# Kernel tuning notes

Measured on AMD Instinct MI355X. Metric: run time of the kernel, lower is better.

## Reference

```python
import jax, jax.numpy as jnp
import numpy as np

B, T, D, H = 32, 1024, 768, 768

def setup_inputs() -> dict:
    key = jax.random.key(0)
    k0, k1, k2, k3 = jax.random.split(key, 4)
    inputs = jax.random.normal(k0, (B, T, D), dtype=jnp.float32)
    # packed-sequence lengths: sorted descending, in [1, T]
    lengths = jnp.sort(jax.random.randint(k1, (B,), 1, T + 1))[::-1]
    # parameters (orthogonal-block init approximated by scaled gaussian)
    W_in = jax.random.normal(k2, (6 * H, D), dtype=jnp.float32) / np.sqrt(D)
    b_in = jnp.zeros((6 * H,), dtype=jnp.float32)
    W_s = jax.random.normal(k3, (5 * H, H), dtype=jnp.float32) / np.sqrt(H)
    # state bias: forget-gate block initialized to 1.0, rest 0
    b_s = jnp.zeros((5 * H,), dtype=jnp.float32).at[H:2 * H].set(1.0)
    return {"inputs": inputs, "W_in": W_in, "b_in": b_in,
            "W_s": W_s, "b_s": b_s, "lengths": lengths}

def reference(inputs, W_in, b_in, W_s, b_s, lengths):
    Bb, Tt, Dd = inputs.shape
    Hh = W_s.shape[1]
    # precompute all input projections in one big GEMM: [B,T,6H]
    proj_in = jnp.einsum('btd,kd->btk', inputs, W_in) + b_in
    mask = jnp.arange(Tt)[None, :] < lengths[:, None]  # [B,T] valid timesteps

    def step(carry, xs):
        h, c = carry                    # [B,H] each
        pi, m = xs                      # pi: [B,6H], m: [B] bool
        ps = h @ W_s.T + b_s            # [B,5H] recurrent GEMM
        i = jax.nn.sigmoid(pi[:, 0*Hh:1*Hh] + ps[:, 0*Hh:1*Hh])
        f = jax.nn.sigmoid(pi[:, 1*Hh:2*Hh] + ps[:, 1*Hh:2*Hh])
        g = jnp.tanh(pi[:, 2*Hh:3*Hh] + ps[:, 2*Hh:3*Hh])
        o = jax.nn.sigmoid(pi[:, 3*Hh:4*Hh] + ps[:, 3*Hh:4*Hh])
        c_new = i * g + f * c
        out = o * jnp.tanh(c_new)
        # highway mix
        hw = jax.nn.sigmoid(pi[:, 4*Hh:5*Hh] + ps[:, 4*Hh:5*Hh])
        out = hw * out + (1.0 - hw) * pi[:, 5*Hh:6*Hh]
        mcol = m[:, None]
        h_next = jnp.where(mcol, out, h)      # freeze state past seq length
        c_next = jnp.where(mcol, c_new, c)
        y = jnp.where(mcol, out, 0.0)          # zero outputs past length
        return (h_next, c_next), y

    h0 = jnp.zeros((Bb, Hh), dtype=inputs.dtype)
    c0 = jnp.zeros((Bb, Hh), dtype=inputs.dtype)
    pi_t = jnp.swapaxes(proj_in, 0, 1)  # [T,B,6H]
    m_t = jnp.swapaxes(mask, 0, 1)      # [T,B]
    (h_fin, c_fin), ys = jax.lax.scan(step, (h0, c0), (pi_t, m_t))
    return jnp.swapaxes(ys, 0, 1)       # [B,T,H]
```

## Files before the change

kernel.cpp:

```cpp
#include <hip/hip_runtime.h>
#include <hip/hip_bf16.h>

#define Bb 32
#define Tt 1024
#define Dd 768
#define Hh 768
#define NGRP 2
#define BPG 96
#define GB  16
#define CPB 8
#define NTHREADS 192

#define NWELE ((size_t)6 * Hh * Dd)
#define NSELE ((size_t)5 * Hh * Hh)
#define WS_NB    4096
#define WS_FLG   8192
#define WS_HBOFF (WS_NB + WS_FLG)
#define HBSZ     (GB * Hh * 2)
#define WS_WGT   (WS_HBOFF + 4 * HBSZ)
#define WS_NEED  (WS_WGT + (NWELE + NSELE) * 2)

typedef short short8 __attribute__((ext_vector_type(8)));
typedef float f4 __attribute__((ext_vector_type(4)));

__device__ __forceinline__ float bf2f(ushort u) {
    unsigned x = (unsigned)u << 16;
    return __builtin_bit_cast(float, x);
}
__device__ __forceinline__ ushort f2bf(float f) {
    unsigned u = __builtin_bit_cast(unsigned, f);
    return (ushort)((u + 0x7fffu + ((u >> 16) & 1u)) >> 16);
}
__device__ __forceinline__ float sigm(float x) { return 1.0f / (1.0f + __expf(-x)); }
__device__ __forceinline__ float tanh_(float x) {
    float e = __expf(2.0f * x);
    return 1.0f - 2.0f / (e + 1.0f);
}

__global__ void prep_nb(const int* __restrict__ len, int* __restrict__ nbArr) {
    int t = blockIdx.x * 256 + threadIdx.x;
    if (t < Tt) {
        int c = 0;
#pragma unroll
        for (int b = 0; b < Bb; ++b) c += (len[b] > t) ? 1 : 0;
        nbArr[t] = c;
    }
}

__global__ void conv_w(const void* __restrict__ Win, const void* __restrict__ Ws,
                       const void* __restrict__ bs, ushort* __restrict__ wOut) {
    const bool isbf = (((const unsigned*)bs)[384] != 0u);
    size_t i = ((size_t)blockIdx.x * 256 + threadIdx.x) * 8;
    if (i >= NWELE + NSELE) return;
    const void* src = (i < NWELE) ? Win : Ws;
    size_t off = (i < NWELE) ? i : (i - NWELE);
    if (isbf) {
        *(uint4*)(wOut + i) = *(const uint4*)((const ushort*)src + off);
    } else {
        const f4* s = (const f4*)((const float*)src + off);
        f4 a = s[0], c = s[1];
        uint4 v;
        v.x = (unsigned)f2bf(a[0]) | ((unsigned)f2bf(a[1]) << 16);
        v.y = (unsigned)f2bf(a[2]) | ((unsigned)f2bf(a[3]) << 16);
        v.z = (unsigned)f2bf(c[0]) | ((unsigned)f2bf(c[1]) << 16);
        v.w = (unsigned)f2bf(c[2]) | ((unsigned)f2bf(c[3]) << 16);
        *(uint4*)(wOut + i) = v;
    }
}

__global__ __launch_bounds__(NTHREADS, 1) void lstm_main(
    const void* __restrict__ inp, const void* __restrict__ bin,
    const void* __restrict__ bs, const int* __restrict__ len,
    void* __restrict__ y, const int* __restrict__ nbArr,
    unsigned* flags, ushort* hbAll, const ushort* __restrict__ wbf)
{
    __shared__ ushort wsL[48 * 776];
    __shared__ ushort hA[GB * 776];
    __shared__ float accT[3][16][16];

    const bool isbf = (((const unsigned*)bs)[384] != 0u);

    const int tid  = threadIdx.x;
    const int lane = tid & 63;
    const int wave = tid >> 6;
    const int g    = blockIdx.x & 1;
    const int w    = blockIdx.x >> 1;
    const int n0   = w * CPB;

    for (int i = tid; i < 48 * 776 / 8; i += NTHREADS)
        *(uint4*)&wsL[i * 8] = uint4{0u, 0u, 0u, 0u};
    const ushort* wbfS = wbf + NWELE;
    __syncthreads();
    for (int i = tid; i < 40 * 96; i += NTHREADS) {
        int c = i / 96, ch = i - c * 96;
        *(uint4*)&wsL[c * 776 + ch * 8] =
            *(const uint4*)(wbfS + ((size_t)((c >> 3) * Hh + n0 + (c & 7))) * Hh + ch * 8);
    }

    float B0 = 0, B1 = 0, B2 = 0, B3 = 0, B4 = 0, B5 = 0, cReg = 0.0f;
    int lenb = 0;
    if (tid < 128) {
        int j = tid & 7, n = n0 + j;
        if (isbf) {
            const ushort* bi = (const ushort*)bin; const ushort* bsp = (const ushort*)bs;
            B0 = bf2f(bi[0 * Hh + n]) + bf2f(bsp[0 * Hh + n]);
            B1 = bf2f(bi[1 * Hh + n]) + bf2f(bsp[1 * Hh + n]);
            B2 = bf2f(bi[2 * Hh + n]) + bf2f(bsp[2 * Hh + n]);
            B3 = bf2f(bi[3 * Hh + n]) + bf2f(bsp[3 * Hh + n]);
            B4 = bf2f(bi[4 * Hh + n]) + bf2f(bsp[4 * Hh + n]);
            B5 = bf2f(bi[5 * Hh + n]);
        } else {
            const float* bi = (const float*)bin; const float* bsp = (const float*)bs;
            B0 = bi[0 * Hh + n] + bsp[0 * Hh + n];
            B1 = bi[1 * Hh + n] + bsp[1 * Hh + n];
            B2 = bi[2 * Hh + n] + bsp[2 * Hh + n];
            B3 = bi[3 * Hh + n] + bsp[3 * Hh + n];
            B4 = bi[4 * Hh + n] + bsp[4 * Hh + n];
            B5 = bi[5 * Hh + n];
        }
        lenb = len[g * GB + (tid >> 3)];
    }

    const int kq = (lane >> 4) << 3;
    const ushort* aP = &hA[(lane & 15) * 776 + kq];
    const int aoff = ((lane >> 4) * 32) + ((lane & 15) * 2);
    const int cc = wave * 16 + (lane & 15);
    const uint4* bPx = (const uint4*)(wbf + ((size_t)((cc >> 3) * Hh + n0 + (cc & 7))) * Dd + kq);
    const ushort* wsP = &wsL[cc * 776 + kq];

    unsigned* wflg = flags + g * 256;
    ushort* hb[2] = {hbAll + (g * 2 + 0) * (HBSZ / 2),
                     hbAll + (g * 2 + 1) * (HBSZ / 2)};
    long gmax = (1L << 22);

    uint4 pfA[8], pfB[8];
    auto pfIssue = [&](int tn) {
        if (isbf) {
            const ushort* xi = (const ushort*)inp;
#pragma unroll
            for (int ii = 0; ii < 8; ++ii) {
                int i = tid + ii * NTHREADS;
                int row = i / 96, c8 = i - row * 96;
                pfA[ii] = *((const uint4*)(xi + ((size_t)(g * GB + row) * Tt + tn) * Dd) + c8);
            }
        } else {
            const float* xf = (const float*)inp;
#pragma unroll
            for (int ii = 0; ii < 8; ++ii) {
                int i = tid + ii * NTHREADS;
                int row = i / 96, c8 = i - row * 96;
                const uint4* s = (const uint4*)(xf + ((size_t)(g * GB + row) * Tt + tn) * Dd + c8 * 8);
                pfA[ii] = s[0]; pfB[ii] = s[1];
            }
        }
    };
    auto pfWrite = [&]() {
        if (isbf) {
#pragma unroll
            for (int ii = 0; ii < 8; ++ii) {
                int i = tid + ii * NTHREADS;
                int row = i / 96, c8 = i - row * 96;
                *(uint4*)&hA[row * 776 + c8 * 8] = pfA[ii];
            }
        } else {
#pragma unroll
            for (int ii = 0; ii < 8; ++ii) {
                int i = tid + ii * NTHREADS;
                int row = i / 96, c8 = i - row * 96;
                float f0 = __builtin_bit_cast(float, pfA[ii].x);
                float f1 = __builtin_bit_cast(float, pfA[ii].y);
                float f2 = __builtin_bit_cast(float, pfA[ii].z);
                float f3 = __builtin_bit_cast(float, pfA[ii].w);
                float f4_ = __builtin_bit_cast(float, pfB[ii].x);
                float f5 = __builtin_bit_cast(float, pfB[ii].y);
                float f6 = __builtin_bit_cast(float, pfB[ii].z);
                float f7 = __builtin_bit_cast(float, pfB[ii].w);
                uint4 v;
                v.x = (unsigned)f2bf(f0) | ((unsigned)f2bf(f1) << 16);
                v.y = (unsigned)f2bf(f2) | ((unsigned)f2bf(f3) << 16);
                v.z = (unsigned)f2bf(f4_) | ((unsigned)f2bf(f5) << 16);
                v.w = (unsigned)f2bf(f6) | ((unsigned)f2bf(f7) << 16);
                *(uint4*)&hA[row * 776 + c8 * 8] = v;
            }
        }
    };

    pfIssue(0);
    pfWrite();
    __syncthreads();

    f4 acc0 = {0, 0, 0, 0}, acc1 = {0, 0, 0, 0};
    f4 acc2 = {0, 0, 0, 0}, acc3 = {0, 0, 0, 0};
#pragma unroll
    for (int kb = 0; kb < 24; ++kb) {
        short8 a = __builtin_bit_cast(short8, *(const uint4*)(aP + kb * 32));
        short8 b = __builtin_bit_cast(short8, bPx[kb * 4]);
        switch (kb & 3) {
        case 0: acc0 = __builtin_amdgcn_mfma_f32_16x16x32_bf16(a, b, acc0, 0, 0, 0); break;
        case 1: acc1 = __builtin_amdgcn_mfma_f32_16x16x32_bf16(a, b, acc1, 0, 0, 0); break;
        case 2: acc2 = __builtin_amdgcn_mfma_f32_16x16x32_bf16(a, b, acc2, 0, 0, 0); break;
        default: acc3 = __builtin_amdgcn_mfma_f32_16x16x32_bf16(a, b, acc3, 0, 0, 0); break;
        }
    }
    pfIssue(1);
    __builtin_amdgcn_sched_barrier(0);

    int tDone = Tt;
    for (int t = 0; t < Tt; ++t) {
        int nbg = nbArr[t] - g * GB;
        nbg = nbg < 0 ? 0 : (nbg > GB ? GB : nbg);
        if (nbg == 0) { tDone = t; break; }

        if (t > 0) {
            const unsigned target = (unsigned)t;
            long guard = 0;
            for (;;) {
                unsigned f0 = __hip_atomic_load(wflg + lane, __ATOMIC_RELAXED,
                                                __HIP_MEMORY_SCOPE_AGENT);
                unsigned f1 = __hip_atomic_load(wflg + 64 + lane, __ATOMIC_RELAXED,
                                                __HIP_MEMORY_SCOPE_AGENT);
                unsigned f2 = __hip_atomic_load(wflg + 128 + lane, __ATOMIC_RELAXED,
                                                __HIP_MEMORY_SCOPE_AGENT);
                bool ok = (f0 >= target) && (f1 >= target) && (f2 >= target);
                if (__all(ok)) break;
                if (++guard > gmax) break;
                __builtin_amdgcn_s_sleep(1);
            }
        }
        __asm__ volatile("" ::: "memory");

        {
            const unsigned long long* aB = (const unsigned long long*)hb[t & 1];
#pragma unroll
            for (int kb = 0; kb < 24; ++kb) {
                unsigned long long v0 = __hip_atomic_load(aB + kb * 128 + aoff,
                                                          __ATOMIC_RELAXED,
                                                          __HIP_MEMORY_SCOPE_AGENT);
                unsigned long long v1 = __hip_atomic_load(aB + kb * 128 + aoff + 1,
                                                          __ATOMIC_RELAXED,
                                                          __HIP_MEMORY_SCOPE_AGENT);
                short8 a;
                __builtin_memcpy(&a, &v0, 8);
                __builtin_memcpy((char*)&a + 8, &v1, 8);
                short8 b = __builtin_bit_cast(short8, *(const uint4*)(wsP + kb * 32));
                switch (kb & 3) {
                case 0: acc0 = __builtin_amdgcn_mfma_f32_16x16x32_bf16(a, b, acc0, 0, 0, 0); break;
                case 1: acc1 = __builtin_amdgcn_mfma_f32_16x16x32_bf16(a, b, acc1, 0, 0, 0); break;
                case 2: acc2 = __builtin_amdgcn_mfma_f32_16x16x32_bf16(a, b, acc2, 0, 0, 0); break;
                default: acc3 = __builtin_amdgcn_mfma_f32_16x16x32_bf16(a, b, acc3, 0, 0, 0); break;
                }
            }
        }
        {
            f4 s = (acc0 + acc1) + (acc2 + acc3);
            int r0 = (lane >> 4) * 4, col = lane & 15;
#pragma unroll
            for (int i = 0; i < 4; ++i) accT[wave][r0 + i][col] = s[i];
        }
        __syncthreads();

        float y0 = 0, y1 = 0, y2 = 0, y3 = 0;
        size_t oiY = 0; bool doY = false;
        if (tid < 128) {
            int b = tid >> 3, j = tid & 7;
            float v0 = accT[(0 * 8 + j) >> 4][b][(0 * 8 + j) & 15];
            float v1 = accT[(1 * 8 + j) >> 4][b][(1 * 8 + j) & 15];
            float v2 = accT[(2 * 8 + j) >> 4][b][(2 * 8 + j) & 15];
            float v3 = accT[(3 * 8 + j) >> 4][b][(3 * 8 + j) & 15];
            float v4 = accT[(4 * 8 + j) >> 4][b][(4 * 8 + j) & 15];
            float v5 = accT[(5 * 8 + j) >> 4][b][(5 * 8 + j) & 15];
            float ii = sigm(v0 + B0);
            float ff = sigm(v1 + B1);
            float gg = tanh_(v2 + B2);
            float oo = sigm(v3 + B3);
            float hw = sigm(v4 + B4);
            float p5 = v5 + B5;
            float cn = ii * gg + ff * cReg;
            float outv = oo * tanh_(cn);
            outv = hw * outv + (1.0f - hw) * p5;
            bool act = t < lenb;
            if (act) cReg = cn;

            int lane6 = tid & 63;
            int g0 = lane6 & ~3;
            float f0v = __shfl(outv, g0 + 0);
            float f1v = __shfl(outv, g0 + 1);
            float f2v = __shfl(outv, g0 + 2);
            float f3v = __shfl(outv, g0 + 3);
            if ((lane6 & 3) == 0) {
                if (act) {
                    unsigned long long vv = (unsigned long long)f2bf(f0v)
                        | ((unsigned long long)f2bf(f1v) << 16)
                        | ((unsigned long long)f2bf(f2v) << 32)
                        | ((unsigned long long)f2bf(f3v) << 48);
                    __hip_atomic_store(
                        (unsigned long long*)(hb[(t & 1) ^ 1] + w * 128 + b * 8 + j),
                        vv, __ATOMIC_RELAXED, __HIP_MEMORY_SCOPE_AGENT);
                }
                doY = true;
                y0 = act ? f0v : 0.0f; y1 = act ? f1v : 0.0f;
                y2 = act ? f2v : 0.0f; y3 = act ? f3v : 0.0f;
                oiY = ((size_t)(g * GB + b) * Tt + t) * Hh + n0 + j;
            }
            __asm__ volatile("s_waitcnt vmcnt(0)" ::: "memory");
            if (lane6 == 0)
                __hip_atomic_store(wflg + w * 2 + wave, (unsigned)(t + 1),
                                   __ATOMIC_RELAXED, __HIP_MEMORY_SCOPE_AGENT);
        }

        if (t + 1 < Tt) pfWrite();
        __syncthreads();

        acc0 = f4{0, 0, 0, 0}; acc1 = f4{0, 0, 0, 0};
        acc2 = f4{0, 0, 0, 0}; acc3 = f4{0, 0, 0, 0};
        if (t + 1 < Tt) {
#pragma unroll
            for (int kb = 0; kb < 24; ++kb) {
                short8 a = __builtin_bit_cast(short8, *(const uint4*)(aP + kb * 32));
                short8 b = __builtin_bit_cast(short8, bPx[kb * 4]);
                switch (kb & 3) {
                case 0: acc0 = __builtin_amdgcn_mfma_f32_16x16x32_bf16(a, b, acc0, 0, 0, 0); break;
                case 1: acc1 = __builtin_amdgcn_mfma_f32_16x16x32_bf16(a, b, acc1, 0, 0, 0); break;
                case 2: acc2 = __builtin_amdgcn_mfma_f32_16x16x32_bf16(a, b, acc2, 0, 0, 0); break;
                default: acc3 = __builtin_amdgcn_mfma_f32_16x16x32_bf16(a, b, acc3, 0, 0, 0); break;
                }
            }
        }
        if (t + 2 < Tt) pfIssue(t + 2);
        __builtin_amdgcn_sched_barrier(0);

        if (doY) {
            if (isbf) {
                unsigned long long vv = (unsigned long long)f2bf(y0)
                    | ((unsigned long long)f2bf(y1) << 16)
                    | ((unsigned long long)f2bf(y2) << 32)
                    | ((unsigned long long)f2bf(y3) << 48);
                *(unsigned long long*)((ushort*)y + oiY) = vv;
            } else {
                *(f4*)((float*)y + oiY) = f4{y0, y1, y2, y3};
            }
        }
    }

    if (tid < 128) {
        int b = tid >> 3, j = tid & 7;
        for (int t = tDone; t < Tt; ++t) {
            size_t oi = ((size_t)(g * GB + b) * Tt + t) * Hh + n0 + j;
            if (isbf) ((ushort*)y)[oi] = 0; else ((float*)y)[oi] = 0.0f;
        }
    }
}

extern "C" void kernel_launch(void* const* d_in, const int* in_sizes, int n_in,
                              void* d_out, int out_size, void* d_ws, size_t ws_size,
                              hipStream_t stream) {
    const void* inp = d_in[0];
    const void* Win = d_in[1];
    const void* bin = d_in[2];
    const void* Ws  = d_in[3];
    const void* bs  = d_in[4];
    const int*  len = (const int*)d_in[5];

    if (ws_size < WS_NEED) return;

    char* ws = (char*)d_ws;
    int* nbArr      = (int*)ws;
    unsigned* flags = (unsigned*)(ws + WS_NB);
    ushort* hbAll   = (ushort*)(ws + WS_HBOFF);
    ushort* wbf     = (ushort*)(ws + WS_WGT);

    hipMemsetAsync(d_ws, 0, WS_WGT, stream);
    prep_nb<<<4, 256, 0, stream>>>(len, nbArr);
    conv_w<<<3168, 256, 0, stream>>>(Win, Ws, bs, wbf);
    lstm_main<<<NGRP * BPG, NTHREADS, 0, stream>>>(inp, bin, bs, len, d_out,
                                                   nbArr, flags, hbAll, wbf);
}
```

Before: 8.660 ms.

## Convert prefetched inputs at issue time, hoist address math, use lighter barriers

The input-prefetch path now precomputes per-thread global and LDS offsets once and converts fp32 to bf16 right when the loads are issued, so the prefetch buffer holds eight packed registers instead of sixteen. The y output store moves to right after the flag publish instead of after the next step's MFMA loop. __syncthreads is replaced with an LDS-only wait plus s_barrier. The aim is to cut register pressure, per-step index arithmetic and barrier cost on the serial recurrence. The cost is that converting at issue time forces an early wait on the global loads, which can stall the step.

Result: slower. 9.295 ms (+7.3%).

```diff
diff --git a/kernel.cpp b/kernel.cpp
--- a/kernel.cpp
+++ b/kernel.cpp
@@ -35,6 +35,24 @@
 __device__ __forceinline__ float tanh_(float x) {
     float e = __expf(2.0f * x);
     return 1.0f - 2.0f / (e + 1.0f);
+}
+__device__ __forceinline__ uint4 packbf(uint4 a, uint4 b) {
+    uint4 v;
+    v.x = (unsigned)f2bf(__builtin_bit_cast(float, a.x))
+        | ((unsigned)f2bf(__builtin_bit_cast(float, a.y)) << 16);
+    v.y = (unsigned)f2bf(__builtin_bit_cast(float, a.z))
+        | ((unsigned)f2bf(__builtin_bit_cast(float, a.w)) << 16);
+    v.z = (unsigned)f2bf(__builtin_bit_cast(float, b.x))
+        | ((unsigned)f2bf(__builtin_bit_cast(float, b.y)) << 16);
+    v.w = (unsigned)f2bf(__builtin_bit_cast(float, b.z))
+        | ((unsigned)f2bf(__builtin_bit_cast(float, b.w)) << 16);
+    return v;
+}
+
+__device__ __forceinline__ void bar_lgkm() {
+    __asm__ volatile("s_waitcnt lgkmcnt(0)" ::: "memory");
+    __builtin_amdgcn_s_barrier();
+    __builtin_amdgcn_sched_barrier(0);
 }
 
 __global__ void prep_nb(const int* __restrict__ len, int* __restrict__ nbArr) {
@@ -133,60 +151,55 @@
                      hbAll + (g * 2 + 1) * (HBSZ / 2)};
     long gmax = (1L << 22);
 
-    uint4 pfA[8], pfB[8];
-    auto pfIssue = [&](int tn) {
-        if (isbf) {
-            const ushort* xi = (const ushort*)inp;
-#pragma unroll
-            for (int ii = 0; ii < 8; ++ii) {
-                int i = tid + ii * NTHREADS;
-                int row = i / 96, c8 = i - row * 96;
-                pfA[ii] = *((const uint4*)(xi + ((size_t)(g * GB + row) * Tt + tn) * Dd) + c8);
-            }
-        } else {
-            const float* xf = (const float*)inp;
-#pragma unroll
-            for (int ii = 0; ii < 8; ++ii) {
-                int i = tid + ii * NTHREADS;
-                int row = i / 96, c8 = i - row * 96;
-                const uint4* s = (const uint4*)(xf + ((size_t)(g * GB + row) * Tt + tn) * Dd + c8 * 8);
-                pfA[ii] = s[0]; pfB[ii] = s[1];
-            }
-        }
-    };
-    auto pfWrite = [&]() {
-        if (isbf) {
-#pragma unroll
-            for (int ii = 0; ii < 8; ++ii) {
-                int i = tid + ii * NTHREADS;
-                int row = i / 96, c8 = i - row * 96;
-                *(uint4*)&hA[row * 776 + c8 * 8] = pfA[ii];
-            }
-        } else {
-#pragma unroll
-            for (int ii = 0; ii < 8; ++ii) {
-                int i = tid + ii * NTHREADS;
-                int row = i / 96, c8 = i - row * 96;
-                float f0 = __builtin_bit_cast(float, pfA[ii].x);
-                float f1 = __builtin_bit_cast(float, pfA[ii].y);
-                float f2 = __builtin_bit_cast(float, pfA[ii].z);
-                float f3 = __builtin_bit_cast(float, pfA[ii].w);
-                float f4_ = __builtin_bit_cast(float, pfB[ii].x);
-                float f5 = __builtin_bit_cast(float, pfB[ii].y);
-                float f6 = __builtin_bit_cast(float, pfB[ii].z);
-                float f7 = __builtin_bit_cast(float, pfB[ii].w);
-                uint4 v;
-                v.x = (unsigned)f2bf(f0) | ((unsigned)f2bf(f1) << 16);
-                v.y = (unsigned)f2bf(f2) | ((unsigned)f2bf(f3) << 16);
-                v.z = (unsigned)f2bf(f4_) | ((unsigned)f2bf(f5) << 16);
-                v.w = (unsigned)f2bf(f6) | ((unsigned)f2bf(f7) << 16);
-                *(uint4*)&hA[row * 776 + c8 * 8] = v;
-            }
-        }
-    };
-
-    pfIssue(0);
-    pfWrite();
+    int r0_ = (tid + 0 * NTHREADS) / 96, c0_ = (tid + 0 * NTHREADS) % 96;
+    int r1_ = (tid + 1 * NTHREADS) / 96, c1_ = (tid + 1 * NTHREADS) % 96;
+    int r2_ = (tid + 2 * NTHREADS) / 96, c2_ = (tid + 2 * NTHREADS) % 96;
+    int r3_ = (tid + 3 * NTHREADS) / 96, c3_ = (tid + 3 * NTHREADS) % 96;
+    int r4_ = (tid + 4 * NTHREADS) / 96, c4_ = (tid + 4 * NTHREADS) % 96;
+    int r5_ = (tid + 5 * NTHREADS) / 96, c5_ = (tid + 5 * NTHREADS) % 96;
+    int r6_ = (tid + 6 * NTHREADS) / 96, c6_ = (tid + 6 * NTHREADS) % 96;
+    int r7_ = (tid + 7 * NTHREADS) / 96, c7_ = (tid + 7 * NTHREADS) % 96;
+    size_t sE0 = ((size_t)(g * GB + r0_) * Tt) * Dd + c0_ * 8;
+    size_t sE1 = ((size_t)(g * GB + r1_) * Tt) * Dd + c1_ * 8;
+    size_t sE2 = ((size_t)(g * GB + r2_) * Tt) * Dd + c2_ * 8;
+    size_t sE3 = ((size_t)(g * GB + r3_) * Tt) * Dd + c3_ * 8;
+    size_t sE4 = ((size_t)(g * GB + r4_) * Tt) * Dd + c4_ * 8;
+    size_t sE5 = ((size_t)(g * GB + r5_) * Tt) * Dd + c5_ * 8;
+    size_t sE6 = ((size_t)(g * GB + r6_) * Tt) * Dd + c6_ * 8;
+    size_t sE7 = ((size_t)(g * GB + r7_) * Tt) * Dd + c7_ * 8;
+    int lo0 = r0_ * 776 + c0_ * 8, lo1 = r1_ * 776 + c1_ * 8;
+    int lo2 = r2_ * 776 + c2_ * 8, lo3 = r3_ * 776 + c3_ * 8;
+    int lo4 = r4_ * 776 + c4_ * 8, lo5 = r5_ * 776 + c5_ * 8;
+    int lo6 = r6_ * 776 + c6_ * 8, lo7 = r7_ * 776 + c7_ * 8;
+
+    uint4 pf0, pf1, pf2, pf3, pf4, pf5, pf6, pf7;
+
+#define PF_ONE(dst, sE, tn) do {                                              \
+        if (isbf) {                                                           \
+            dst = *(const uint4*)((const ushort*)inp + sE + (size_t)(tn) * Dd); \
+        } else {                                                              \
+            const uint4* s_ = (const uint4*)((const float*)inp + sE + (size_t)(tn) * Dd); \
+            uint4 a_ = s_[0], b_ = s_[1];                                     \
+            dst = packbf(a_, b_);                                             \
+        }                                                                     \
+    } while (0)
+
+#define PF_ISSUE(tn) do {                                                     \
+        PF_ONE(pf0, sE0, tn); PF_ONE(pf1, sE1, tn);                           \
+        PF_ONE(pf2, sE2, tn); PF_ONE(pf3, sE3, tn);                           \
+        PF_ONE(pf4, sE4, tn); PF_ONE(pf5, sE5, tn);                           \
+        PF_ONE(pf6, sE6, tn); PF_ONE(pf7, sE7, tn);                           \
+    } while (0)
+
+#define PF_WRITE() do {                                                       \
+        *(uint4*)&hA[lo0] = pf0; *(uint4*)&hA[lo1] = pf1;                     \
+        *(uint4*)&hA[lo2] = pf2; *(uint4*)&hA[lo3] = pf3;                     \
+        *(uint4*)&hA[lo4] = pf4; *(uint4*)&hA[lo5] = pf5;                     \
+        *(uint4*)&hA[lo6] = pf6; *(uint4*)&hA[lo7] = pf7;                     \
+    } while (0)
+
+    PF_ISSUE(0);
+    PF_WRITE();
     __syncthreads();
 
     f4 acc0 = {0, 0, 0, 0}, acc1 = {0, 0, 0, 0};
@@ -202,7 +215,7 @@
         default: acc3 = __builtin_amdgcn_mfma_f32_16x16x32_bf16(a, b, acc3, 0, 0, 0); break;
         }
     }
-    pfIssue(1);
+    PF_ISSUE(1);
     __builtin_amdgcn_sched_barrier(0);
 
     int tDone = Tt;
@@ -257,10 +270,8 @@
 #pragma unroll
             for (int i = 0; i < 4; ++i) accT[wave][r0 + i][col] = s[i];
         }
-        __syncthreads();
-
-        float y0 = 0, y1 = 0, y2 = 0, y3 = 0;
-        size_t oiY = 0; bool doY = false;
+        bar_lgkm();
+
         if (tid < 128) {
             int b = tid >> 3, j = tid & 7;
             float v0 = accT[(0 * 8 + j) >> 4][b][(0 * 8 + j) & 15];
@@ -287,29 +298,38 @@
             float f1v = __shfl(outv, g0 + 1);
             float f2v = __shfl(outv, g0 + 2);
             float f3v = __shfl(outv, g0 + 3);
-            if ((lane6 & 3) == 0) {
-                if (act) {
-                    unsigned long long vv = (unsigned long long)f2bf(f0v)
-                        | ((unsigned long long)f2bf(f1v) << 16)
-                        | ((unsigned long long)f2bf(f2v) << 32)
-                        | ((unsigned long long)f2bf(f3v) << 48);
-                    __hip_atomic_store(
-                        (unsigned long long*)(hb[(t & 1) ^ 1] + w * 128 + b * 8 + j),
-                        vv, __ATOMIC_RELAXED, __HIP_MEMORY_SCOPE_AGENT);
-                }
-                doY = true;
-                y0 = act ? f0v : 0.0f; y1 = act ? f1v : 0.0f;
-                y2 = act ? f2v : 0.0f; y3 = act ? f3v : 0.0f;
-                oiY = ((size_t)(g * GB + b) * Tt + t) * Hh + n0 + j;
+            if ((lane6 & 3) == 0 && act) {
+                unsigned long long vv = (unsigned long long)f2bf(f0v)
+                    | ((unsigned long long)f2bf(f1v) << 16)
+                    | ((unsigned long long)f2bf(f2v) << 32)
+                    | ((unsigned long long)f2bf(f3v) << 48);
+                __hip_atomic_store(
+                    (unsigned long long*)(hb[(t & 1) ^ 1] + w * 128 + b * 8 + j),
+                    vv, __ATOMIC_RELAXED, __HIP_MEMORY_SCOPE_AGENT);
             }
             __asm__ volatile("s_waitcnt vmcnt(0)" ::: "memory");
             if (lane6 == 0)
                 __hip_atomic_store(wflg + w * 2 + wave, (unsigned)(t + 1),
                                    __ATOMIC_RELAXED, __HIP_MEMORY_SCOPE_AGENT);
-        }
-
-        if (t + 1 < Tt) pfWrite();
-        __syncthreads();
+
+            if ((lane6 & 3) == 0) {
+                size_t oiY = ((size_t)(g * GB + b) * Tt + t) * Hh + n0 + j;
+                float y0 = act ? f0v : 0.0f, y1 = act ? f1v : 0.0f;
+                float y2 = act ? f2v : 0.0f, y3 = act ? f3v : 0.0f;
+                if (isbf) {
+                    unsigned long long vv = (unsigned long long)f2bf(y0)
+                        | ((unsigned long long)f2bf(y1) << 16)
+                        | ((unsigned long long)f2bf(y2) << 32)
+                        | ((unsigned long long)f2bf(y3) << 48);
+                    *(unsigned long long*)((ushort*)y + oiY) = vv;
+                } else {
+                    *(f4*)((float*)y + oiY) = f4{y0, y1, y2, y3};
+                }
+            }
+        }
+
+        if (t + 1 < Tt) PF_WRITE();
+        bar_lgkm();
 
         acc0 = f4{0, 0, 0, 0}; acc1 = f4{0, 0, 0, 0};
         acc2 = f4{0, 0, 0, 0}; acc3 = f4{0, 0, 0, 0};
@@ -326,20 +346,8 @@
                 }
             }
         }
-        if (t + 2 < Tt) pfIssue(t + 2);
+        if (t + 2 < Tt) PF_ISSUE(t + 2);
         __builtin_amdgcn_sched_barrier(0);
-
-        if (doY) {
-            if (isbf) {
-                unsigned long long vv = (unsigned long long)f2bf(y0)
-                    | ((unsigned long long)f2bf(y1) << 16)
-                    | ((unsigned long long)f2bf(y2) << 32)
-                    | ((unsigned long long)f2bf(y3) << 48);
-                *(unsigned long long*)((ushort*)y + oiY) = vv;
-            } else {
-                *(f4*)((float*)y + oiY) = f4{y0, y1, y2, y3};
-            }
-        }
     }
 
     if (tid < 128) {
```
